# Performance work log

Measured on AMD Instinct MI355X. Metric: run time of the kernel, lower is better.

The kernel has to match this reference:

```python
import jax, jax.numpy as jnp
import numpy as np

NUM_NODES = 100000
EMBED_DIM = 64
NUM_EDGES = 1200000
NUM_LAYERS = 3
ALPHA = 0.25  # 1 / (num_layers + 1)


def setup_inputs() -> dict:
    key = jax.random.key(0)
    k1, k2, k3, k4 = jax.random.split(key, 4)
    x = jax.random.normal(k1, (NUM_NODES, EMBED_DIM), dtype=jnp.float32)
    edge_attr = jax.random.uniform(k2, (NUM_EDGES,), dtype=jnp.float32)
    edge_index = jax.random.randint(k3, (2, NUM_EDGES), 0, NUM_NODES, dtype=jnp.int64)
    edge_mask = jax.random.randint(k4, (NUM_EDGES,), 0, 2, dtype=jnp.int32).astype(jnp.bool_)
    return {"x": x, "edge_attr": edge_attr, "edge_index": edge_index, "edge_mask": edge_mask}


def reference(x, edge_attr, edge_index, edge_mask):
    # Masked edge selection == zeroing masked edge weights (same degree & aggregation).
    w = edge_attr * edge_mask.astype(edge_attr.dtype)  # [E]
    row, col = edge_index[0], edge_index[1]            # source, target

    # gcn_norm with add_self_loops=False: D^{-1/2} A D^{-1/2}
    deg = jax.ops.segment_sum(w, col, num_segments=NUM_NODES)          # [N]
    dinv = jnp.where(deg > 0, jax.lax.rsqrt(deg), 0.0)                 # [N]
    norm = dinv[row] * w * dinv[col]                                   # [E]

    out = ALPHA * x
    h = x
    for _ in range(NUM_LAYERS):
        msg = norm[:, None] * h[row]                                   # [E, D] gather
        h = jax.ops.segment_sum(msg, col, num_segments=NUM_NODES)      # [N, D] scatter
        out = out + ALPHA * h
    return out
```

## Files before the change

### kernel.cpp

```cpp
#include <hip/hip_runtime.h>
#include <hip/hip_fp16.h>

#define N_NODES 100000
#define EMB     64
#define N_EDGES 1200000
#define ALPHA   0.25f
#define SCAN_CHUNK 1024
#define NPART ((N_NODES + SCAN_CHUNK - 1) / SCAN_CHUNK)

__global__ __launch_bounds__(256) void k_prep(
        const float4* __restrict__ x4, float4* __restrict__ x16,
        const unsigned char* __restrict__ maskB, const int* __restrict__ idx,
        int* __restrict__ flags) {
    int tid = blockIdx.x * blockDim.x + threadIdx.x;
    if (tid < 16384) {
        int lane = threadIdx.x & 63;
        bool mev = (tid & 3) && maskB[tid];
        if (__any(mev) && lane == 0) atomicOr(&flags[0], 1);
        bool iev = (tid < 4096) && (idx[2 * tid + 1] != 0);
        if (__any(iev) && lane == 0) atomicOr(&flags[1], 1);
    }
    size_t b = (size_t)tid * 2;
    float4 v0 = x4[b], v1 = x4[b + 1];
    float4 o;
    __half2* op = reinterpret_cast<__half2*>(&o);
    op[0] = __floats2half2_rn(v0.x, v0.y);
    op[1] = __floats2half2_rn(v0.z, v0.w);
    op[2] = __floats2half2_rn(v1.x, v1.y);
    op[3] = __floats2half2_rn(v1.z, v1.w);
    x16[tid] = o;
}

__device__ __forceinline__ int idx_row(const int* idx, int i64, int e) {
    return i64 ? idx[2 * e] : idx[e];
}
__device__ __forceinline__ int idx_col(const int* idx, int i64, int e) {
    return i64 ? idx[2 * (N_EDGES + e)] : idx[N_EDGES + e];
}
__device__ __forceinline__ int edge_mask(const void* maskp, int mbool, int e) {
    return mbool ? (int)((const unsigned char*)maskp)[e] : ((const int*)maskp)[e];
}

__global__ void k_hist(const float* __restrict__ ea, const void* maskp,
                       const int* __restrict__ idx, const int* __restrict__ flags,
                       int* __restrict__ cnt, float* __restrict__ degf,
                       int* __restrict__ rank) {
    int e = blockIdx.x * blockDim.x + threadIdx.x;
    if (e >= N_EDGES) return;
    int mbool = flags[0] != 0, i64 = (flags[1] == 0);
    if (!edge_mask(maskp, mbool, e)) return;
    float wv = ea[e];
    if (wv == 0.0f) return;
    int c = idx_col(idx, i64, e);
    if ((unsigned)c >= N_NODES) return;
    rank[e] = atomicAdd(&cnt[c], 1);
    atomicAdd(&degf[c], wv);
}

__global__ void k_scanx(const int* __restrict__ cnt, const float* __restrict__ degf,
                        int* __restrict__ gTotal, int* __restrict__ row_start,
                        float* __restrict__ dinv) {
    __shared__ int sh[256];
    __shared__ int sbase;
    int tid = threadIdx.x;
    int base = blockIdx.x * SCAN_CHUNK + tid * 4;
    int v[4];
    int s = 0;
#pragma unroll
    for (int k = 0; k < 4; ++k) {
        int i = base + k;
        if (i < N_NODES) {
            v[k] = cnt[i];
            float dg = degf[i];
            dinv[i] = (dg > 0.0f) ? rsqrtf(dg) : 0.0f;
        } else {
            v[k] = 0;
        }
        s += v[k];
    }
    sh[tid] = s;
    __syncthreads();
    for (int d = 1; d < 256; d <<= 1) {
        int t = (tid >= d) ? sh[tid - d] : 0;
        __syncthreads();
        sh[tid] += t;
        __syncthreads();
    }
    if (tid == 255) sbase = atomicAdd(gTotal, sh[255]);
    __syncthreads();
    int off = sbase + sh[tid] - s;
#pragma unroll
    for (int k = 0; k < 4; ++k) {
        int i = base + k;
        if (i < N_NODES) { row_start[i] = off; off += v[k]; }
    }
}

__global__ void k_fill(const float* __restrict__ ea, const void* maskp,
                       const int* __restrict__ idx, const int* __restrict__ flags,
                       const int* __restrict__ row_start, const int* __restrict__ rank,
                       const float* __restrict__ dinv, int2* __restrict__ csr) {
    int e = blockIdx.x * blockDim.x + threadIdx.x;
    if (e >= N_EDGES) return;
    int mbool = flags[0] != 0, i64 = (flags[1] == 0);
    if (!edge_mask(maskp, mbool, e)) return;
    float wv = ea[e];
    if (wv == 0.0f) return;
    int c = idx_col(idx, i64, e);
    if ((unsigned)c >= N_NODES) return;
    int r = idx_row(idx, i64, e);
    int rok = (unsigned)r < N_NODES;
    int rc = rok ? r : 0;
    float wn = rok ? wv * dinv[c] * dinv[rc] : 0.0f;
    int p = row_start[c] + rank[e];
    if ((unsigned)p < N_EDGES)
        csr[p] = make_int2(__float_as_int(wn), rc);
}

__device__ __forceinline__ void slice_bounds(const int* row_start, const int* cnt,
                                             int n, int& beg, int& end) {
    beg = row_start[n];
    if (beg < 0) beg = 0;
    if (beg > N_EDGES) beg = N_EDGES;
    int c = cnt[n];
    if (c < 0) c = 0;
    end = beg + c;
    if (end > N_EDGES) end = N_EDGES;
}

__device__ __forceinline__ void accum_h8(float4& sa, float4& sb, float w,
                                         float4 raw) {
    const __half2* hp = reinterpret_cast<const __half2*>(&raw);
    float2 f0 = __half22float2(hp[0]);
    float2 f1 = __half22float2(hp[1]);
    float2 f2 = __half22float2(hp[2]);
    float2 f3 = __half22float2(hp[3]);
    sa.x += w * f0.x; sa.y += w * f0.y; sa.z += w * f1.x; sa.w += w * f1.y;
    sb.x += w * f2.x; sb.y += w * f2.y; sb.z += w * f3.x; sb.w += w * f3.y;
}

__device__ __forceinline__ void gather_core_f16(
        const int* __restrict__ row_start, const int* __restrict__ cnt,
        const int2* __restrict__ csr, const float4* __restrict__ h16,
        int n, int q, float4& sa, float4& sb) {
    int beg, end;
    slice_bounds(row_start, cnt, n, beg, end);
    sa = make_float4(0.f, 0.f, 0.f, 0.f);
    sb = make_float4(0.f, 0.f, 0.f, 0.f);
    for (int j = beg; j < end; j += 4) {
        int last = end - 1;
        int j1 = j + 1 < last ? j + 1 : last;
        int j2 = j + 2 < last ? j + 2 : last;
        int j3 = j + 3 < last ? j + 3 : last;
        int2 p0 = csr[j];
        int2 p1 = csr[j1];
        int2 p2 = csr[j2];
        int2 p3 = csr[j3];
        bool a1 = j + 1 < end, a2 = j + 2 < end, a3 = j + 3 < end;
        float w0 = __int_as_float(p0.x);
        float w1 = a1 ? __int_as_float(p1.x) : 0.0f;
        float w2 = a2 ? __int_as_float(p2.x) : 0.0f;
        float w3 = a3 ? __int_as_float(p3.x) : 0.0f;
        int r0 = min((unsigned)p0.y, (unsigned)(N_NODES - 1));
        int r1 = a1 ? min((unsigned)p1.y, (unsigned)(N_NODES - 1)) : 0;
        int r2 = a2 ? min((unsigned)p2.y, (unsigned)(N_NODES - 1)) : 0;
        int r3 = a3 ? min((unsigned)p3.y, (unsigned)(N_NODES - 1)) : 0;
        float4 v0 = h16[(size_t)r0 * 8 + q];
        float4 v1 = h16[(size_t)r1 * 8 + q];
        float4 v2 = h16[(size_t)r2 * 8 + q];
        float4 v3 = h16[(size_t)r3 * 8 + q];
        accum_h8(sa, sb, w0, v0);
        accum_h8(sa, sb, w1, v1);
        accum_h8(sa, sb, w2, v2);
        accum_h8(sa, sb, w3, v3);
    }
}

__global__ __launch_bounds__(256) void k_gather_mid(
        const int* __restrict__ row_start, const int* __restrict__ cnt,
        const int2* __restrict__ csr,
        const float4* __restrict__ hsrc16, float4* __restrict__ hdst16) {
    int t = blockIdx.x * blockDim.x + threadIdx.x;
    int n = t >> 3;
    int q = t & 7;
    if (n >= N_NODES) return;
    float4 sa, sb;
    gather_core_f16(row_start, cnt, csr, hsrc16, n, q, sa, sb);
    float4 o;
    __half2* op = reinterpret_cast<__half2*>(&o);
    op[0] = __floats2half2_rn(sa.x, sa.y);
    op[1] = __floats2half2_rn(sa.z, sa.w);
    op[2] = __floats2half2_rn(sb.x, sb.y);
    op[3] = __floats2half2_rn(sb.z, sb.w);
    hdst16[(size_t)n * 8 + q] = o;
}

__global__ __launch_bounds__(256) void k_gather_last(
        const int* __restrict__ row_start, const int* __restrict__ cnt,
        const int2* __restrict__ csr,
        const float4* __restrict__ x4, const float4* __restrict__ h1_16,
        const float4* __restrict__ h2_16, float4* __restrict__ out4) {
    int t = blockIdx.x * blockDim.x + threadIdx.x;
    int n = t >> 3;
    int q = t & 7;
    if (n >= N_NODES) return;
    float4 sa, sb;
    gather_core_f16(row_start, cnt, csr, h2_16, n, q, sa, sb);
    size_t o8 = (size_t)n * 8 + q;
    float4 r1 = h1_16[o8];
    float4 r2 = h2_16[o8];
    const __half2* a1 = reinterpret_cast<const __half2*>(&r1);
    const __half2* a2 = reinterpret_cast<const __half2*>(&r2);
    float2 b10 = __half22float2(a1[0]), b11 = __half22float2(a1[1]);
    float2 b12 = __half22float2(a1[2]), b13 = __half22float2(a1[3]);
    float2 b20 = __half22float2(a2[0]), b21 = __half22float2(a2[1]);
    float2 b22 = __half22float2(a2[2]), b23 = __half22float2(a2[3]);
    size_t ox = (size_t)n * 16 + 2 * q;
    float4 x0 = x4[ox], x1 = x4[ox + 1];
    float4 o0, o1;
    o0.x = ALPHA * (x0.x + b10.x + b20.x + sa.x);
    o0.y = ALPHA * (x0.y + b10.y + b20.y + sa.y);
    o0.z = ALPHA * (x0.z + b11.x + b21.x + sa.z);
    o0.w = ALPHA * (x0.w + b11.y + b21.y + sa.w);
    o1.x = ALPHA * (x1.x + b12.x + b22.x + sb.x);
    o1.y = ALPHA * (x1.y + b12.y + b22.y + sb.y);
    o1.z = ALPHA * (x1.z + b13.x + b23.x + sb.z);
    o1.w = ALPHA * (x1.w + b13.y + b23.y + sb.w);
    out4[ox] = o0;
    out4[ox + 1] = o1;
}

extern "C" void kernel_launch(void* const* d_in, const int* in_sizes, int n_in,
                              void* d_out, int out_size, void* d_ws, size_t ws_size,
                              hipStream_t stream) {
    const float* x   = (const float*)d_in[0];
    const float* ea  = (const float*)d_in[1];
    const int*   idx = (const int*)d_in[2];
    const void*  msk = d_in[3];
    float*       out = (float*)d_out;

    char* ws = (char*)d_ws;
    size_t off = 0;
    auto alloc = [&](size_t bytes) -> void* {
        void* p = ws + off;
        off = (off + bytes + 255) & ~(size_t)255;
        return p;
    };
    int*    flags     = (int*)   alloc(64);
    int*    cnt       = (int*)   alloc(sizeof(int)   * N_NODES);
    float*  degf      = (float*) alloc(sizeof(float) * N_NODES);
    int*    row_start = (int*)   alloc(sizeof(int)   * N_NODES);
    float*  dinv      = (float*) alloc(sizeof(float) * N_NODES);
    int*    rank      = (int*)   alloc(sizeof(int)   * N_EDGES);
    int2*   csr       = (int2*)  alloc(sizeof(int2)  * N_EDGES);
    float4* x16       = (float4*)alloc(sizeof(unsigned short) * (size_t)N_NODES * EMB);
    float4* hA16      = (float4*)alloc(sizeof(unsigned short) * (size_t)N_NODES * EMB);
    float4* hB16      = (float4*)alloc(sizeof(unsigned short) * (size_t)N_NODES * EMB);
    int*    gTotal    = flags + 8;

    const int B = 256;
    const int gE = (N_EDGES + B - 1) / B;
    const int gP = (N_NODES * EMB / 8 + B - 1) / B;
    const int gG = (N_NODES * 8 + B - 1) / B;

    (void)hipMemsetAsync(flags, 0, (size_t)((char*)row_start - (char*)flags), stream);
    k_prep <<<gP, B, 0, stream>>>((const float4*)x, x16,
                                  (const unsigned char*)msk, idx, flags);
    k_hist <<<gE, B, 0, stream>>>(ea, msk, idx, flags, cnt, degf, rank);
    k_scanx<<<NPART, 256, 0, stream>>>(cnt, degf, gTotal, row_start, dinv);
    k_fill <<<gE, B, 0, stream>>>(ea, msk, idx, flags, row_start, rank, dinv, csr);

    k_gather_mid <<<gG, B, 0, stream>>>(row_start, cnt, csr, x16,  hA16);
    k_gather_mid <<<gG, B, 0, stream>>>(row_start, cnt, csr, hA16, hB16);
    k_gather_last<<<gG, B, 0, stream>>>(row_start, cnt, csr, (const float4*)x,
                                        hA16, hB16, (float4*)out);
}
```

Measured before the change: 220.6 us.

## Factor symmetric normalization into node scaling and compute degree from CSR

Removes the float atomicAdd degree histogram and the per-edge dinv gathers in the fill kernel. CSR now stores raw weights, and a new per-node kernel sums each node's CSR segment to get the degree, dinv and sqrt(deg). The same kernel scales x by dinv into fp16. The propagation then runs on a rescaled variable t = D^{-1/2} h, with per-node d^2 scaling after each gather and rescaling by sqrt(deg) and dinv in the final combine. This adds a kernel launch and one extra pass over the CSR, and changes the fp16 value ranges, which could affect precision.

```diff
diff --git a/kernel.cpp b/kernel.cpp
--- a/kernel.cpp
+++ b/kernel.cpp
@@ -8,27 +8,14 @@
 #define SCAN_CHUNK 1024
 #define NPART ((N_NODES + SCAN_CHUNK - 1) / SCAN_CHUNK)
 
-__global__ __launch_bounds__(256) void k_prep(
-        const float4* __restrict__ x4, float4* __restrict__ x16,
-        const unsigned char* __restrict__ maskB, const int* __restrict__ idx,
-        int* __restrict__ flags) {
+__global__ void k_detect(const unsigned char* __restrict__ maskB,
+                         const int* __restrict__ idx, int* __restrict__ flags) {
     int tid = blockIdx.x * blockDim.x + threadIdx.x;
-    if (tid < 16384) {
-        int lane = threadIdx.x & 63;
-        bool mev = (tid & 3) && maskB[tid];
-        if (__any(mev) && lane == 0) atomicOr(&flags[0], 1);
-        bool iev = (tid < 4096) && (idx[2 * tid + 1] != 0);
-        if (__any(iev) && lane == 0) atomicOr(&flags[1], 1);
-    }
-    size_t b = (size_t)tid * 2;
-    float4 v0 = x4[b], v1 = x4[b + 1];
-    float4 o;
-    __half2* op = reinterpret_cast<__half2*>(&o);
-    op[0] = __floats2half2_rn(v0.x, v0.y);
-    op[1] = __floats2half2_rn(v0.z, v0.w);
-    op[2] = __floats2half2_rn(v1.x, v1.y);
-    op[3] = __floats2half2_rn(v1.z, v1.w);
-    x16[tid] = o;
+    int lane = threadIdx.x & 63;
+    bool mev = (tid & 3) && maskB[tid];
+    if (__any(mev) && lane == 0) atomicOr(&flags[0], 1);
+    bool iev = (tid < 4096) && (idx[2 * tid + 1] != 0);
+    if (__any(iev) && lane == 0) atomicOr(&flags[1], 1);
 }
 
 __device__ __forceinline__ int idx_row(const int* idx, int i64, int e) {
@@ -43,8 +30,7 @@
 
 __global__ void k_hist(const float* __restrict__ ea, const void* maskp,
                        const int* __restrict__ idx, const int* __restrict__ flags,
-                       int* __restrict__ cnt, float* __restrict__ degf,
-                       int* __restrict__ rank) {
+                       int* __restrict__ cnt, int* __restrict__ rank) {
     int e = blockIdx.x * blockDim.x + threadIdx.x;
     if (e >= N_EDGES) return;
     int mbool = flags[0] != 0, i64 = (flags[1] == 0);
@@ -54,12 +40,10 @@
     int c = idx_col(idx, i64, e);
     if ((unsigned)c >= N_NODES) return;
     rank[e] = atomicAdd(&cnt[c], 1);
-    atomicAdd(&degf[c], wv);
-}
-
-__global__ void k_scanx(const int* __restrict__ cnt, const float* __restrict__ degf,
-                        int* __restrict__ gTotal, int* __restrict__ row_start,
-                        float* __restrict__ dinv) {
+}
+
+__global__ void k_scanx(const int* __restrict__ cnt, int* __restrict__ gTotal,
+                        int* __restrict__ row_start) {
     __shared__ int sh[256];
     __shared__ int sbase;
     int tid = threadIdx.x;
@@ -69,13 +53,7 @@
 #pragma unroll
     for (int k = 0; k < 4; ++k) {
         int i = base + k;
-        if (i < N_NODES) {
-            v[k] = cnt[i];
-            float dg = degf[i];
-            dinv[i] = (dg > 0.0f) ? rsqrtf(dg) : 0.0f;
-        } else {
-            v[k] = 0;
-        }
+        v[k] = (i < N_NODES) ? cnt[i] : 0;
         s += v[k];
     }
     sh[tid] = s;
@@ -99,7 +77,7 @@
 __global__ void k_fill(const float* __restrict__ ea, const void* maskp,
                        const int* __restrict__ idx, const int* __restrict__ flags,
                        const int* __restrict__ row_start, const int* __restrict__ rank,
-                       const float* __restrict__ dinv, int2* __restrict__ csr) {
+                       int2* __restrict__ csr) {
     int e = blockIdx.x * blockDim.x + threadIdx.x;
     if (e >= N_EDGES) return;
     int mbool = flags[0] != 0, i64 = (flags[1] == 0);
@@ -110,11 +88,9 @@
     if ((unsigned)c >= N_NODES) return;
     int r = idx_row(idx, i64, e);
     int rok = (unsigned)r < N_NODES;
-    int rc = rok ? r : 0;
-    float wn = rok ? wv * dinv[c] * dinv[rc] : 0.0f;
     int p = row_start[c] + rank[e];
     if ((unsigned)p < N_EDGES)
-        csr[p] = make_int2(__float_as_int(wn), rc);
+        csr[p] = make_int2(__float_as_int(rok ? wv : 0.0f), rok ? r : 0);
 }
 
 __device__ __forceinline__ void slice_bounds(const int* row_start, const int* cnt,
@@ -126,6 +102,37 @@
     if (c < 0) c = 0;
     end = beg + c;
     if (end > N_EDGES) end = N_EDGES;
+}
+
+__global__ __launch_bounds__(256) void k_degconv(
+        const int* __restrict__ row_start, const int* __restrict__ cnt,
+        const int2* __restrict__ csr, const float4* __restrict__ x4,
+        float4* __restrict__ t0, float* __restrict__ dinv, float* __restrict__ sd) {
+    int t = blockIdx.x * blockDim.x + threadIdx.x;
+    int n = t >> 3;
+    int q = t & 7;
+    if (n >= N_NODES) return;
+    int beg, end;
+    slice_bounds(row_start, cnt, n, beg, end);
+    float s = 0.0f;
+    for (int j = beg + q; j < end; j += 8) s += __int_as_float(csr[j].x);
+    s += __shfl_xor(s, 1);
+    s += __shfl_xor(s, 2);
+    s += __shfl_xor(s, 4);
+    float di = (s > 0.0f) ? rsqrtf(s) : 0.0f;
+    if (q == 0) {
+        dinv[n] = di;
+        sd[n] = (s > 0.0f) ? sqrtf(s) : 0.0f;
+    }
+    size_t xb = (size_t)n * 16 + q * 2;
+    float4 v0 = x4[xb], v1 = x4[xb + 1];
+    float4 o;
+    __half2* op = reinterpret_cast<__half2*>(&o);
+    op[0] = __floats2half2_rn(di * v0.x, di * v0.y);
+    op[1] = __floats2half2_rn(di * v0.z, di * v0.w);
+    op[2] = __floats2half2_rn(di * v1.x, di * v1.y);
+    op[3] = __floats2half2_rn(di * v1.z, di * v1.w);
+    t0[(size_t)n * 8 + q] = o;
 }
 
 __device__ __forceinline__ void accum_h8(float4& sa, float4& sb, float w,
@@ -178,37 +185,42 @@
 
 __global__ __launch_bounds__(256) void k_gather_mid(
         const int* __restrict__ row_start, const int* __restrict__ cnt,
-        const int2* __restrict__ csr,
-        const float4* __restrict__ hsrc16, float4* __restrict__ hdst16) {
+        const int2* __restrict__ csr, const float* __restrict__ dinv,
+        const float4* __restrict__ tsrc, float4* __restrict__ tdst) {
     int t = blockIdx.x * blockDim.x + threadIdx.x;
     int n = t >> 3;
     int q = t & 7;
     if (n >= N_NODES) return;
     float4 sa, sb;
-    gather_core_f16(row_start, cnt, csr, hsrc16, n, q, sa, sb);
+    gather_core_f16(row_start, cnt, csr, tsrc, n, q, sa, sb);
+    float di = dinv[n];
+    float d2 = di * di;
     float4 o;
     __half2* op = reinterpret_cast<__half2*>(&o);
-    op[0] = __floats2half2_rn(sa.x, sa.y);
-    op[1] = __floats2half2_rn(sa.z, sa.w);
-    op[2] = __floats2half2_rn(sb.x, sb.y);
-    op[3] = __floats2half2_rn(sb.z, sb.w);
-    hdst16[(size_t)n * 8 + q] = o;
+    op[0] = __floats2half2_rn(d2 * sa.x, d2 * sa.y);
+    op[1] = __floats2half2_rn(d2 * sa.z, d2 * sa.w);
+    op[2] = __floats2half2_rn(d2 * sb.x, d2 * sb.y);
+    op[3] = __floats2half2_rn(d2 * sb.z, d2 * sb.w);
+    tdst[(size_t)n * 8 + q] = o;
 }
 
 __global__ __launch_bounds__(256) void k_gather_last(
         const int* __restrict__ row_start, const int* __restrict__ cnt,
-        const int2* __restrict__ csr,
-        const float4* __restrict__ x4, const float4* __restrict__ h1_16,
-        const float4* __restrict__ h2_16, float4* __restrict__ out4) {
+        const int2* __restrict__ csr, const float* __restrict__ dinv,
+        const float* __restrict__ sd,
+        const float4* __restrict__ x4, const float4* __restrict__ t1_16,
+        const float4* __restrict__ t2_16, float4* __restrict__ out4) {
     int t = blockIdx.x * blockDim.x + threadIdx.x;
     int n = t >> 3;
     int q = t & 7;
     if (n >= N_NODES) return;
     float4 sa, sb;
-    gather_core_f16(row_start, cnt, csr, h2_16, n, q, sa, sb);
+    gather_core_f16(row_start, cnt, csr, t2_16, n, q, sa, sb);
+    float di = dinv[n];
+    float sdv = sd[n];
     size_t o8 = (size_t)n * 8 + q;
-    float4 r1 = h1_16[o8];
-    float4 r2 = h2_16[o8];
+    float4 r1 = t1_16[o8];
+    float4 r2 = t2_16[o8];
     const __half2* a1 = reinterpret_cast<const __half2*>(&r1);
     const __half2* a2 = reinterpret_cast<const __half2*>(&r2);
     float2 b10 = __half22float2(a1[0]), b11 = __half22float2(a1[1]);
@@ -218,14 +230,14 @@
     size_t ox = (size_t)n * 16 + 2 * q;
     float4 x0 = x4[ox], x1 = x4[ox + 1];
     float4 o0, o1;
-    o0.x = ALPHA * (x0.x + b10.x + b20.x + sa.x);
-    o0.y = ALPHA * (x0.y + b10.y + b20.y + sa.y);
-    o0.z = ALPHA * (x0.z + b11.x + b21.x + sa.z);
-    o0.w = ALPHA * (x0.w + b11.y + b21.y + sa.w);
-    o1.x = ALPHA * (x1.x + b12.x + b22.x + sb.x);
-    o1.y = ALPHA * (x1.y + b12.y + b22.y + sb.y);
-    o1.z = ALPHA * (x1.z + b13.x + b23.x + sb.z);
-    o1.w = ALPHA * (x1.w + b13.y + b23.y + sb.w);
+    o0.x = ALPHA * (x0.x + sdv * (b10.x + b20.x) + di * sa.x);
+    o0.y = ALPHA * (x0.y + sdv * (b10.y + b20.y) + di * sa.y);
+    o0.z = ALPHA * (x0.z + sdv * (b11.x + b21.x) + di * sa.z);
+    o0.w = ALPHA * (x0.w + sdv * (b11.y + b21.y) + di * sa.w);
+    o1.x = ALPHA * (x1.x + sdv * (b12.x + b22.x) + di * sb.x);
+    o1.y = ALPHA * (x1.y + sdv * (b12.y + b22.y) + di * sb.y);
+    o1.z = ALPHA * (x1.z + sdv * (b13.x + b23.x) + di * sb.z);
+    o1.w = ALPHA * (x1.w + sdv * (b13.y + b23.y) + di * sb.w);
     out4[ox] = o0;
     out4[ox + 1] = o1;
 }
@@ -248,30 +260,30 @@
     };
     int*    flags     = (int*)   alloc(64);
     int*    cnt       = (int*)   alloc(sizeof(int)   * N_NODES);
-    float*  degf      = (float*) alloc(sizeof(float) * N_NODES);
     int*    row_start = (int*)   alloc(sizeof(int)   * N_NODES);
     float*  dinv      = (float*) alloc(sizeof(float) * N_NODES);
+    float*  sd        = (float*) alloc(sizeof(float) * N_NODES);
     int*    rank      = (int*)   alloc(sizeof(int)   * N_EDGES);
     int2*   csr       = (int2*)  alloc(sizeof(int2)  * N_EDGES);
-    float4* x16       = (float4*)alloc(sizeof(unsigned short) * (size_t)N_NODES * EMB);
-    float4* hA16      = (float4*)alloc(sizeof(unsigned short) * (size_t)N_NODES * EMB);
-    float4* hB16      = (float4*)alloc(sizeof(unsigned short) * (size_t)N_NODES * EMB);
+    float4* t0        = (float4*)alloc(sizeof(unsigned short) * (size_t)N_NODES * EMB);
+    float4* tA        = (float4*)alloc(sizeof(unsigned short) * (size_t)N_NODES * EMB);
+    float4* tB        = (float4*)alloc(sizeof(unsigned short) * (size_t)N_NODES * EMB);
     int*    gTotal    = flags + 8;
 
     const int B = 256;
     const int gE = (N_EDGES + B - 1) / B;
-    const int gP = (N_NODES * EMB / 8 + B - 1) / B;
     const int gG = (N_NODES * 8 + B - 1) / B;
 
     (void)hipMemsetAsync(flags, 0, (size_t)((char*)row_start - (char*)flags), stream);
-    k_prep <<<gP, B, 0, stream>>>((const float4*)x, x16,
-                                  (const unsigned char*)msk, idx, flags);
-    k_hist <<<gE, B, 0, stream>>>(ea, msk, idx, flags, cnt, degf, rank);
-    k_scanx<<<NPART, 256, 0, stream>>>(cnt, degf, gTotal, row_start, dinv);
-    k_fill <<<gE, B, 0, stream>>>(ea, msk, idx, flags, row_start, rank, dinv, csr);
-
-    k_gather_mid <<<gG, B, 0, stream>>>(row_start, cnt, csr, x16,  hA16);
-    k_gather_mid <<<gG, B, 0, stream>>>(row_start, cnt, csr, hA16, hB16);
-    k_gather_last<<<gG, B, 0, stream>>>(row_start, cnt, csr, (const float4*)x,
-                                        hA16, hB16, (float4*)out);
-}
+    k_detect <<<64, 256, 0, stream>>>((const unsigned char*)msk, idx, flags);
+    k_hist   <<<gE, B, 0, stream>>>(ea, msk, idx, flags, cnt, rank);
+    k_scanx  <<<NPART, 256, 0, stream>>>(cnt, gTotal, row_start);
+    k_fill   <<<gE, B, 0, stream>>>(ea, msk, idx, flags, row_start, rank, csr);
+    k_degconv<<<gG, B, 0, stream>>>(row_start, cnt, csr, (const float4*)x,
+                                    t0, dinv, sd);
+
+    k_gather_mid <<<gG, B, 0, stream>>>(row_start, cnt, csr, dinv, t0, tA);
+    k_gather_mid <<<gG, B, 0, stream>>>(row_start, cnt, csr, dinv, tA, tB);
+    k_gather_last<<<gG, B, 0, stream>>>(row_start, cnt, csr, dinv, sd,
+                                        (const float4*)x, tA, tB, (float4*)out);
+}
```

After: 191.8 us. -13.1%, faster.
